# Optimization experiments

Measured on AMD Instinct MI355X. Metric: run time of the kernel, lower is better.

## Reference

```python
import jax, jax.numpy as jnp
import numpy as np

B, T, D, H, L, V = 4, 1024, 1024, 16, 6, 32000
HS = D // H
FF = 4 * D
EPS = 1e-5


def setup_inputs() -> dict:
    key = jax.random.key(0)
    ks = jax.random.split(key, 16)
    s = 0.02
    n = lambda k, shape: (jax.random.normal(k, shape, jnp.float32) * s)
    return {
        'idx': jax.random.randint(ks[0], (B, T), 0, V),
        'targets': jax.random.randint(ks[1], (B, T), 0, V),
        'tok_emb': n(ks[2], (V, D)),
        'pos_emb': n(ks[3], (T, D)),
        'Wq': n(ks[4], (L, D, H, HS)),
        'Wk': n(ks[5], (L, D, H, HS)),
        'Wv': n(ks[6], (L, D, H, HS)),
        'proj_w': n(ks[7], (L, D, D)),
        'proj_b': jnp.zeros((L, D), jnp.float32),
        'ln1_g': jnp.ones((L, D), jnp.float32),
        'ln1_b': jnp.zeros((L, D), jnp.float32),
        'ln2_g': jnp.ones((L, D), jnp.float32),
        'ln2_b': jnp.zeros((L, D), jnp.float32),
        'ff_w1': n(ks[8], (L, D, FF)),
        'ff_b1': jnp.zeros((L, FF), jnp.float32),
        'ff_w2': n(ks[9], (L, FF, D)),
        'ff_b2': jnp.zeros((L, D), jnp.float32),
        'lnf_g': jnp.ones((D,), jnp.float32),
        'lnf_b': jnp.zeros((D,), jnp.float32),
        'head_w': n(ks[10], (D, V)),
        'head_b': jnp.zeros((V,), jnp.float32),
    }


def _ln(x, g, b):
    m = jnp.mean(x, axis=-1, keepdims=True)
    v = jnp.mean((x - m) ** 2, axis=-1, keepdims=True)
    return (x - m) * jax.lax.rsqrt(v + EPS) * g + b


def _forward(idx, targets, tok_emb, pos_emb, Wq, Wk, Wv, proj_w, proj_b,
             ln1_g, ln1_b, ln2_g, ln2_b, ff_w1, ff_b1, ff_w2, ff_b2,
             lnf_g, lnf_b, head_w, head_b):
    b, t = idx.shape
    x = tok_emb[idx] + pos_emb[:t]                       # [B,T,D]
    mask = jnp.tril(jnp.ones((t, t), bool))              # causal
    scale = jnp.float32(D) ** -0.5                       # NOTE: scales by num_dims (c), as in source
    for l in range(L):
        h = _ln(x, ln1_g[l], ln1_b[l])
        q = jnp.einsum('btd,dhs->bhts', h, Wq[l])        # [B,H,T,HS]
        k = jnp.einsum('btd,dhs->bhts', h, Wk[l])
        v = jnp.einsum('btd,dhs->bhts', h, Wv[l])
        w = jnp.einsum('bhts,bhus->bhtu', q, k) * scale  # [B,H,T,T]
        w = jnp.where(mask, w, -jnp.inf)
        w = jax.nn.softmax(w, axis=-1)
        o = jnp.einsum('bhtu,bhus->bhts', w, v)          # [B,H,T,HS]
        o = o.transpose(0, 2, 1, 3).reshape(b, t, D)     # concat heads
        x = x + jnp.einsum('btd,de->bte', o, proj_w[l]) + proj_b[l]
        h2 = _ln(x, ln2_g[l], ln2_b[l])
        ff = jax.nn.relu(jnp.einsum('btd,df->btf', h2, ff_w1[l]) + ff_b1[l])
        x = x + jnp.einsum('btf,fd->btd', ff, ff_w2[l]) + ff_b2[l]
    x = _ln(x, lnf_g, lnf_b)
    logits = jnp.einsum('btd,dv->btv', x, head_w) + head_b
    logits = logits.reshape(b * t, V)
    tgt = targets.reshape(b * t)
    logp = jax.nn.log_softmax(logits, axis=-1)
    loss = -jnp.mean(jnp.take_along_axis(logp, tgt[:, None], axis=-1))
    return logits, loss


def reference(idx, targets, tok_emb, pos_emb, Wq, Wk, Wv, proj_w, proj_b,
              ln1_g, ln1_b, ln2_g, ln2_b, ff_w1, ff_b1, ff_w2, ff_b2,
              lnf_g, lnf_b, head_w, head_b):
    return _forward(idx, targets, tok_emb, pos_emb, Wq, Wk, Wv, proj_w, proj_b,
                    ln1_g, ln1_b, ln2_g, ln2_b, ff_w1, ff_b1, ff_w2, ff_b2,
                    lnf_g, lnf_b, head_w, head_b)
```

## Files before the change

### kernel.cpp

```cpp
#include <hip/hip_runtime.h>

typedef __attribute__((ext_vector_type(8))) short bf16x8;
typedef __attribute__((ext_vector_type(4))) float f32x4;

#define L_LAYERS 6
#define T_SEQ 1024
#define D_MODEL 1024
#define N_HEAD 16
#define HS 64
#define FF_DIM 4096
#define VOCAB 32000
#define BT_ROWS 4096
#define ATTN_SCALE 0.03125f

__device__ __forceinline__ ushort f2bf(float f) {
  unsigned u = __builtin_bit_cast(unsigned, f);
  unsigned r = (u + 0x7fffu + ((u >> 16) & 1u)) >> 16;
  return (ushort)r;
}
__device__ __forceinline__ float waveRedSum(float v) {
#pragma unroll
  for (int off = 32; off; off >>= 1) v += __shfl_xor(v, off);
  return v;
}
__device__ __forceinline__ void gload16(const void* g, void* l) {
  __builtin_amdgcn_global_load_lds(
      (const __attribute__((address_space(1))) unsigned int*)g,
      (__attribute__((address_space(3))) unsigned int*)l, 16, 0, 0);
}

__global__ __launch_bounds__(256) void embed_kernel(const int* __restrict__ idx,
                                                    const float* __restrict__ tok,
                                                    const float* __restrict__ pos,
                                                    float* __restrict__ x) {
  int row = blockIdx.x;
  int tid = threadIdx.x;
  int t = row & (T_SEQ - 1);
  int id = idx[row];
  float4 tv = ((const float4*)(tok + (size_t)id * D_MODEL))[tid];
  float4 pv = ((const float4*)(pos + (size_t)t * D_MODEL))[tid];
  tv.x += pv.x; tv.y += pv.y; tv.z += pv.z; tv.w += pv.w;
  ((float4*)(x + (size_t)row * D_MODEL))[tid] = tv;
}

__global__ __launch_bounds__(256) void ln_kernel(const float* __restrict__ x,
                                                 const float* __restrict__ g,
                                                 const float* __restrict__ b,
                                                 ushort* __restrict__ out) {
  int row = blockIdx.x;
  int tid = threadIdx.x;
  __shared__ float red[4];
  float4 xv = ((const float4*)(x + (size_t)row * D_MODEL))[tid];
  float s = xv.x + xv.y + xv.z + xv.w;
  s = waveRedSum(s);
  if ((tid & 63) == 0) red[tid >> 6] = s;
  __syncthreads();
  float mean = (red[0] + red[1] + red[2] + red[3]) * (1.0f / D_MODEL);
  __syncthreads();
  float d0 = xv.x - mean, d1 = xv.y - mean, d2 = xv.z - mean, d3 = xv.w - mean;
  float v = d0 * d0 + d1 * d1 + d2 * d2 + d3 * d3;
  v = waveRedSum(v);
  if ((tid & 63) == 0) red[tid >> 6] = v;
  __syncthreads();
  float var = (red[0] + red[1] + red[2] + red[3]) * (1.0f / D_MODEL);
  float rstd = rsqrtf(var + 1e-5f);
  float4 gv = ((const float4*)g)[tid];
  float4 bv = ((const float4*)b)[tid];
  ushort4 o;
  o.x = f2bf(d0 * rstd * gv.x + bv.x);
  o.y = f2bf(d1 * rstd * gv.y + bv.y);
  o.z = f2bf(d2 * rstd * gv.z + bv.z);
  o.w = f2bf(d3 * rstd * gv.w + bv.w);
  ((ushort4*)(out + (size_t)row * D_MODEL))[tid] = o;
}

__device__ __forceinline__ void wconv_body(const float* __restrict__ W,
                                           ushort* __restrict__ WT,
                                           int Kd, int Nd, int n0, int k0) {
  __shared__ ushort tile[64][72];
  int tid = threadIdx.x;
#pragma unroll
  for (int i = 0; i < 4; i++) {
    int c = tid + i * 256;
    int row = c >> 4, cc = c & 15;
    float4 wv = *(const float4*)&W[(size_t)(k0 + row) * Nd + n0 + cc * 4];
    tile[row][cc * 4 + 0] = f2bf(wv.x);
    tile[row][cc * 4 + 1] = f2bf(wv.y);
    tile[row][cc * 4 + 2] = f2bf(wv.z);
    tile[row][cc * 4 + 3] = f2bf(wv.w);
  }
  __syncthreads();
#pragma unroll
  for (int i = 0; i < 2; i++) {
    int c = tid + i * 256;
    int n = c >> 3, kc = c & 7;
    __align__(16) ushort tmp[8];
#pragma unroll
    for (int j = 0; j < 8; j++) tmp[j] = tile[kc * 8 + j][n];
    *(int4*)&WT[(size_t)(n0 + n) * Kd + k0 + kc * 8] = *(const int4*)tmp;
  }
}

__global__ __launch_bounds__(256) void wconv_kernel(const float* __restrict__ W,
                                                    ushort* __restrict__ WT,
                                                    int Kd, int Nd) {
  wconv_body(W, WT, Kd, Nd, blockIdx.x * 64, blockIdx.y * 64);
}

__global__ __launch_bounds__(256) void wconv4_kernel(const float* __restrict__ W0,
                                                     const float* __restrict__ W1,
                                                     const float* __restrict__ W2,
                                                     const float* __restrict__ W3,
                                                     ushort* __restrict__ WT,
                                                     int Kd, int Nd) {
  int z = blockIdx.z;
  const float* W = (z == 0) ? W0 : (z == 1) ? W1 : (z == 2) ? W2 : W3;
  wconv_body(W, WT + (size_t)z * Kd * Nd, Kd, Nd, blockIdx.x * 64, blockIdx.y * 64);
}

__global__ __launch_bounds__(256) void vtrans_kernel(const ushort* __restrict__ v,
                                                     ushort* __restrict__ vT) {
  __shared__ ushort tile[64][72];
  int bh = blockIdx.y;
  int t0 = blockIdx.x * 64;
  int tid = threadIdx.x;
#pragma unroll
  for (int i = 0; i < 2; i++) {
    int c = tid + i * 256;
    int row = c >> 3, cc = c & 7;
    *(int4*)&tile[row][cc * 8] =
        *(const int4*)&v[((size_t)bh * T_SEQ + t0 + row) * HS + cc * 8];
  }
  __syncthreads();
#pragma unroll
  for (int i = 0; i < 2; i++) {
    int c = tid + i * 256;
    int hs = c >> 3, tc = c & 7;
    __align__(16) ushort tmp[8];
#pragma unroll
    for (int j = 0; j < 8; j++) tmp[j] = tile[tc * 8 + j][hs];
    *(int4*)&vT[((size_t)bh * HS + hs) * T_SEQ + t0 + tc * 8] = *(const int4*)tmp;
  }
}

template <int BM, int BN, int WM, int WN, int EPI>
__global__ __launch_bounds__(WM * WN * 64, 2) void gemmp_kernel(
    const ushort* __restrict__ A, const ushort* __restrict__ BT, int K,
    const float* __restrict__ bias, float* __restrict__ outf,
    ushort* __restrict__ outb, ushort* __restrict__ outk,
    ushort* __restrict__ outv, int ldo) {
  constexpr int PM = BM / WM, PN = BN / WN;
  constexpr int MR = PM / 16, NR = PN / 16;
  constexpr int ROWS = BM + BN;
  constexpr int NWAVES = WM * WN;
  constexpr int LPW = (ROWS / 8) / NWAVES;
  __shared__ __align__(16) ushort buf[2][ROWS * 64];
  int tid = threadIdx.x;
  int lane = tid & 63, wave = tid >> 6;
  int wm = wave / WN, wn = wave % WN;
  int a = lane & 15, gg = lane >> 4;
  int srow8 = lane >> 3;
  int scol8 = ((lane & 7) ^ (lane >> 3)) * 8;
  int m0 = blockIdx.y * BM, n0 = blockIdx.x * BN;
  f32x4 acc[MR][NR] = {};
  int nt = K >> 6;

  auto STAGE = [&](int t, int d) {
    int k0 = t * 64;
#pragma unroll
    for (int j = 0; j < LPW; j++) {
      int r0 = (wave * LPW + j) * 8;
      if (r0 < BM) {
        gload16(&A[(size_t)(m0 + r0 + srow8) * K + k0 + scol8], &buf[d][r0 * 64]);
      } else {
        gload16(&BT[(size_t)(n0 + (r0 - BM) + srow8) * K + k0 + scol8], &buf[d][r0 * 64]);
      }
    }
  };

  auto COMPUTE = [&](int d) {
    const ushort* bA = &buf[d][0];
    const ushort* bB = &buf[d][BM * 64];
#pragma unroll
    for (int s = 0; s < 2; s++) {
      bf16x8 af[MR], bfr[NR];
#pragma unroll
      for (int i = 0; i < MR; i++) {
        int row = wm * PM + i * 16 + a;
        af[i] = *(const bf16x8*)&bA[row * 64 + (((s * 4 + gg) ^ (a & 7)) * 8)];
      }
#pragma unroll
      for (int j = 0; j < NR; j++) {
        int row = wn * PN + j * 16 + a;
        bfr[j] = *(const bf16x8*)&bB[row * 64 + (((s * 4 + gg) ^ (a & 7)) * 8)];
      }
#pragma unroll
      for (int i = 0; i < MR; i++)
#pragma unroll
        for (int j = 0; j < NR; j++)
          acc[i][j] = __builtin_amdgcn_mfma_f32_16x16x32_bf16(af[i], bfr[j], acc[i][j], 0, 0, 0);
    }
  };

  STAGE(0, 0);
  __syncthreads();
  int cur = 0;
  for (int t = 0; t < nt; t++) {
    if (t + 1 < nt) STAGE(t + 1, cur ^ 1);
    COMPUTE(cur);
    __syncthreads();
    cur ^= 1;
  }

#pragma unroll
  for (int i = 0; i < MR; i++) {
#pragma unroll
    for (int j = 0; j < NR; j++) {
#pragma unroll
      for (int r = 0; r < 4; r++) {
        int mrow = m0 + wm * PM + i * 16 + gg * 4 + r;
        int ncol = n0 + wn * PN + j * 16 + a;
        float v = acc[i][j][r];
        if (EPI == 0) {
          int which = ncol >> 10;
          int n1 = ncol & 1023;
          int h = n1 >> 6, sidx = n1 & 63;
          int bb = mrow >> 10, tt = mrow & 1023;
          ushort* dst = (which == 0) ? outb : (which == 1) ? outk : outv;
          dst[(((size_t)(bb * N_HEAD + h)) * T_SEQ + tt) * HS + sidx] = f2bf(v);
        } else if (EPI == 1) {
          outf[(size_t)mrow * ldo + ncol] += v + bias[ncol];
        } else if (EPI == 2) {
          float t2 = v + bias[ncol];
          outb[(size_t)mrow * ldo + ncol] = f2bf(t2 > 0.0f ? t2 : 0.0f);
        } else {
          outf[(size_t)mrow * ldo + ncol] = v + bias[ncol];
        }
      }
    }
  }
}

template <int EPI, bool SWZ>
__global__ __launch_bounds__(512, 2) void gemm8_kernel(
    const ushort* __restrict__ A, const ushort* __restrict__ BT, int K,
    const float* __restrict__ bias, float* __restrict__ outf,
    ushort* __restrict__ outb, ushort* __restrict__ outk,
    ushort* __restrict__ outv, int ldo) {
  extern __shared__ __align__(16) ushort lds[];
  int tid = threadIdx.x;
  int lane = tid & 63, wave = tid >> 6;
  int wm = wave >> 2, wn = wave & 3;
  int a = lane & 15, gg = lane >> 4;
  int bx = blockIdx.x, by = blockIdx.y;
  if (SWZ) {
    int gx = gridDim.x, nwg = gx * gridDim.y;
    int wg = by * gx + bx;
    int id = (wg & 7) * (nwg >> 3) + (wg >> 3);
    bx = id % gx; by = id / gx;
  }
  int m0 = by * 256, n0 = bx * 256;
  int srow = lane >> 3;
  int scol = ((lane & 7) ^ (lane >> 3)) * 8;
  int nt = K >> 6;
  f32x4 acc[8][4] = {};

  auto stageHalf = [&](int t, int which) {
    int d = t & 1;
    int k0 = t * 64;
    const ushort* src = (which < 2) ? A : BT;
    int base0 = ((which < 2) ? m0 : n0) + (which & 1) * 128;
    ushort* dst = lds + ((which < 2) ? 0 : 32768) + d * 16384 + (which & 1) * 8192;
#pragma unroll
    for (int q = 0; q < 2; q++) {
      int r0 = q * 64 + wave * 8;
      gload16(&src[(size_t)(base0 + r0 + srow) * K + k0 + scol], dst + r0 * 64);
    }
  };

  stageHalf(0, 0); stageHalf(0, 1); stageHalf(0, 2); stageHalf(0, 3);
  if (nt > 1) {
    stageHalf(1, 2); stageHalf(1, 3);
    asm volatile("s_waitcnt vmcnt(4)" ::: "memory");
  } else {
    asm volatile("s_waitcnt vmcnt(0)" ::: "memory");
  }
  __builtin_amdgcn_sched_barrier(0);
  __builtin_amdgcn_s_barrier();

  for (int t = 0; t < nt; t++) {
    int d = t & 1;
    const ushort* bA = lds + d * 16384;
    const ushort* bB = lds + 32768 + d * 16384;
    bf16x8 alo[4][2], ahi[4][2], bj01[2][2], bj23[2][2];
#pragma unroll
    for (int i = 0; i < 4; i++)
#pragma unroll
      for (int s = 0; s < 2; s++) {
        int row = wm * 128 + i * 16 + a;
        alo[i][s] = *(const bf16x8*)&bA[row * 64 + (((s * 4 + gg) ^ (a & 7)) * 8)];
      }
#pragma unroll
    for (int j = 0; j < 2; j++)
#pragma unroll
      for (int s = 0; s < 2; s++) {
        int row = wn * 64 + j * 16 + a;
        bj01[j][s] = *(const bf16x8*)&bB[row * 64 + (((s * 4 + gg) ^ (a & 7)) * 8)];
      }
    if (t + 1 < nt) stageHalf(t + 1, 0);
    __builtin_amdgcn_s_barrier();
    asm volatile("s_waitcnt lgkmcnt(0)" ::: "memory");
    __builtin_amdgcn_sched_barrier(0);
    __builtin_amdgcn_s_setprio(1);
#pragma unroll
    for (int i = 0; i < 4; i++)
#pragma unroll
      for (int j = 0; j < 2; j++)
#pragma unroll
        for (int s = 0; s < 2; s++)
          acc[i][j] = __builtin_amdgcn_mfma_f32_16x16x32_bf16(alo[i][s], bj01[j][s], acc[i][j], 0, 0, 0);
    __builtin_amdgcn_s_setprio(0);
    __builtin_amdgcn_s_barrier();
#pragma unroll
    for (int j = 0; j < 2; j++)
#pragma unroll
      for (int s = 0; s < 2; s++) {
        int row = wn * 64 + (j + 2) * 16 + a;
        bj23[j][s] = *(const bf16x8*)&bB[row * 64 + (((s * 4 + gg) ^ (a & 7)) * 8)];
      }
    if (t + 1 < nt) stageHalf(t + 1, 1);
    __builtin_amdgcn_s_barrier();
    asm volatile("s_waitcnt lgkmcnt(0)" ::: "memory");
    __builtin_amdgcn_sched_barrier(0);
    __builtin_amdgcn_s_setprio(1);
#pragma unroll
    for (int i = 0; i < 4; i++)
#pragma unroll
      for (int j = 0; j < 2; j++)
#pragma unroll
        for (int s = 0; s < 2; s++)
          acc[i][j + 2] = __builtin_amdgcn_mfma_f32_16x16x32_bf16(alo[i][s], bj23[j][s], acc[i][j + 2], 0, 0, 0);
    __builtin_amdgcn_s_setprio(0);
    __builtin_amdgcn_s_barrier();
#pragma unroll
    for (int i = 0; i < 4; i++)
#pragma unroll
      for (int s = 0; s < 2; s++) {
        int row = wm * 128 + (i + 4) * 16 + a;
        ahi[i][s] = *(const bf16x8*)&bA[row * 64 + (((s * 4 + gg) ^ (a & 7)) * 8)];
      }
    if (t + 2 < nt) stageHalf(t + 2, 2);
    __builtin_amdgcn_s_barrier();
    asm volatile("s_waitcnt lgkmcnt(0)" ::: "memory");
    __builtin_amdgcn_sched_barrier(0);
    __builtin_amdgcn_s_setprio(1);
#pragma unroll
    for (int i = 0; i < 4; i++)
#pragma unroll
      for (int j = 0; j < 2; j++)
#pragma unroll
        for (int s = 0; s < 2; s++)
          acc[i + 4][j] = __builtin_amdgcn_mfma_f32_16x16x32_bf16(ahi[i][s], bj01[j][s], acc[i + 4][j], 0, 0, 0);
    __builtin_amdgcn_s_setprio(0);
    __builtin_amdgcn_s_barrier();
    if (t + 2 < nt) stageHalf(t + 2, 3);
    __builtin_amdgcn_s_barrier();
    __builtin_amdgcn_s_setprio(1);
#pragma unroll
    for (int i = 0; i < 4; i++)
#pragma unroll
      for (int j = 0; j < 2; j++)
#pragma unroll
        for (int s = 0; s < 2; s++)
          acc[i + 4][j + 2] = __builtin_amdgcn_mfma_f32_16x16x32_bf16(ahi[i][s], bj23[j][s], acc[i + 4][j + 2], 0, 0, 0);
    __builtin_amdgcn_s_setprio(0);
    __builtin_amdgcn_sched_barrier(0);
    if (t + 1 < nt) {
      if (t + 2 < nt) asm volatile("s_waitcnt vmcnt(4)" ::: "memory");
      else            asm volatile("s_waitcnt vmcnt(0)" ::: "memory");
      __builtin_amdgcn_sched_barrier(0);
    }
    __builtin_amdgcn_s_barrier();
  }

#pragma unroll
  for (int i = 0; i < 8; i++) {
#pragma unroll
    for (int j = 0; j < 4; j++) {
#pragma unroll
      for (int r = 0; r < 4; r++) {
        int mrow = m0 + wm * 128 + i * 16 + gg * 4 + r;
        int ncol = n0 + wn * 64 + j * 16 + a;
        float v = acc[i][j][r];
        if (EPI == 0) {
          int which = ncol >> 10;
          int n1 = ncol & 1023;
          int h = n1 >> 6, sidx = n1 & 63;
          int bb = mrow >> 10, tt = mrow & 1023;
          ushort* dst = (which == 0) ? outb : (which == 1) ? outk : outv;
          dst[(((size_t)(bb * N_HEAD + h)) * T_SEQ + tt) * HS + sidx] = f2bf(v);
        } else if (EPI == 2) {
          float t2 = v + bias[ncol];
          outb[(size_t)mrow * ldo + ncol] = f2bf(t2 > 0.0f ? t2 : 0.0f);
        } else {
          outf[(size_t)mrow * ldo + ncol] = v + bias[ncol];
        }
      }
    }
  }
}

__global__ __launch_bounds__(256) void attn_kernel(const ushort* __restrict__ q,
                                                   const ushort* __restrict__ k,
                                                   const ushort* __restrict__ vT,
                                                   ushort* __restrict__ o) {
  __shared__ __align__(16) ushort Ksm[64 * 72];
  __shared__ __align__(16) ushort Vsm[64 * 72];
  __shared__ __align__(16) ushort Psm[4][16 * 72];
  int tid = threadIdx.x;
  int lane = tid & 63, w = tid >> 6;
  int a = lane & 15, gg = lane >> 4;
  int qt = blockIdx.x, bh = blockIdx.y;
  int qrow_b = qt * 64 + w * 16;
  int qmy = qrow_b + a;

  bf16x8 qf[2];
  const ushort* qbase = q + ((size_t)bh * T_SEQ + qmy) * HS;
  qf[0] = *(const bf16x8*)&qbase[gg * 8];
  qf[1] = *(const bf16x8*)&qbase[32 + gg * 8];

  float m_run = -__builtin_inff();
  float l_run = 0.0f;
  f32x4 oacc[4] = {};
  int nkt = qt + 1;

  for (int kt = 0; kt < nkt; kt++) {
    int k0 = kt * 64;
    __syncthreads();
#pragma unroll
    for (int i = 0; i < 2; i++) {
      int c = tid + i * 256;
      int row = c >> 3, cc = c & 7;
      *(int4*)&Ksm[row * 72 + cc * 8] =
          *(const int4*)&k[((size_t)bh * T_SEQ + k0 + row) * HS + cc * 8];
      *(int4*)&Vsm[row * 72 + cc * 8] =
          *(const int4*)&vT[((size_t)bh * HS + row) * T_SEQ + k0 + cc * 8];
    }
    __syncthreads();

    f32x4 st[4] = {};
#pragma unroll
    for (int ku = 0; ku < 4; ku++) {
#pragma unroll
      for (int s = 0; s < 2; s++) {
        bf16x8 kf = *(const bf16x8*)&Ksm[(ku * 16 + a) * 72 + s * 32 + gg * 8];
        st[ku] = __builtin_amdgcn_mfma_f32_16x16x32_bf16(kf, qf[s], st[ku], 0, 0, 0);
      }
    }

    float pv[16];
    float pm = -__builtin_inff();
#pragma unroll
    for (int ku = 0; ku < 4; ku++) {
#pragma unroll
      for (int r = 0; r < 4; r++) {
        int u = k0 + ku * 16 + gg * 4 + r;
        float val = (u <= qmy) ? st[ku][r] * ATTN_SCALE : -__builtin_inff();
        pv[ku * 4 + r] = val;
        pm = fmaxf(pm, val);
      }
    }
    pm = fmaxf(pm, __shfl_xor(pm, 16));
    pm = fmaxf(pm, __shfl_xor(pm, 32));
    float m_new = fmaxf(m_run, pm);
    float cfac = expf(m_run - m_new);
    float tsum = 0.0f;
#pragma unroll
    for (int xi = 0; xi < 16; xi++) {
      float p = expf(pv[xi] - m_new);
      pv[xi] = p;
      tsum += p;
    }
    tsum += __shfl_xor(tsum, 16);
    tsum += __shfl_xor(tsum, 32);
    l_run = l_run * cfac + tsum;
    m_run = m_new;

    ushort* P = (ushort*)&Psm[w][0];
    asm volatile("s_waitcnt lgkmcnt(0)" ::: "memory");
#pragma unroll
    for (int ku = 0; ku < 4; ku++) {
      ushort4 pw;
      pw.x = f2bf(pv[ku * 4 + 0]);
      pw.y = f2bf(pv[ku * 4 + 1]);
      pw.z = f2bf(pv[ku * 4 + 2]);
      pw.w = f2bf(pv[ku * 4 + 3]);
      *(ushort4*)&P[a * 72 + ku * 16 + gg * 4] = pw;
    }
#pragma unroll
    for (int r = 0; r < 4; r++) {
      float cr = __shfl(cfac, gg * 4 + r);
#pragma unroll
      for (int nb = 0; nb < 4; nb++) oacc[nb][r] *= cr;
    }
    asm volatile("s_waitcnt lgkmcnt(0)" ::: "memory");
#pragma unroll
    for (int kb = 0; kb < 2; kb++) {
      bf16x8 pa = *(const bf16x8*)&P[a * 72 + kb * 32 + gg * 8];
#pragma unroll
      for (int nb = 0; nb < 4; nb++) {
        bf16x8 vb = *(const bf16x8*)&Vsm[(nb * 16 + a) * 72 + kb * 32 + gg * 8];
        oacc[nb] = __builtin_amdgcn_mfma_f32_16x16x32_bf16(pa, vb, oacc[nb], 0, 0, 0);
      }
    }
  }

  float linv = 1.0f / l_run;
  int bb = bh >> 4, hh = bh & 15;
#pragma unroll
  for (int r = 0; r < 4; r++) {
    float li = __shfl(linv, gg * 4 + r);
    int qr = qrow_b + gg * 4 + r;
#pragma unroll
    for (int nb = 0; nb < 4; nb++) {
      o[((size_t)(bb * T_SEQ + qr)) * D_MODEL + hh * HS + nb * 16 + a] =
          f2bf(oacc[nb][r] * li);
    }
  }
}

__global__ __launch_bounds__(256) void loss_row_kernel(const float* __restrict__ logits,
                                                       const int* __restrict__ tgt,
                                                       float* __restrict__ row_loss) {
  int row = blockIdx.x, tid = threadIdx.x;
  __shared__ float redm[4], reds[4];
  const float4* l4 = (const float4*)(logits + (size_t)row * VOCAB);
  float m = -__builtin_inff(), s = 0.0f;
  for (int i = tid; i < VOCAB / 4; i += 256) {
    float4 v = l4[i];
    float cm = fmaxf(fmaxf(v.x, v.y), fmaxf(v.z, v.w));
    if (cm > m) { s *= expf(m - cm); m = cm; }
    s += expf(v.x - m) + expf(v.y - m) + expf(v.z - m) + expf(v.w - m);
  }
#pragma unroll
  for (int off = 32; off; off >>= 1) {
    float om = __shfl_xor(m, off), os = __shfl_xor(s, off);
    float nm = fmaxf(m, om);
    s = s * expf(m - nm) + os * expf(om - nm);
    m = nm;
  }
  if ((tid & 63) == 0) { redm[tid >> 6] = m; reds[tid >> 6] = s; }
  __syncthreads();
  if (tid == 0) {
    float M = fmaxf(fmaxf(redm[0], redm[1]), fmaxf(redm[2], redm[3]));
    float S = reds[0] * expf(redm[0] - M) + reds[1] * expf(redm[1] - M) +
              reds[2] * expf(redm[2] - M) + reds[3] * expf(redm[3] - M);
    row_loss[row] = M + logf(S) - logits[(size_t)row * VOCAB + tgt[row]];
  }
}

__global__ __launch_bounds__(256) void loss_final_kernel(const float* __restrict__ row_loss,
                                                         float* __restrict__ out) {
  int tid = threadIdx.x;
  __shared__ float red[4];
  float s = 0.0f;
  for (int i = tid; i < BT_ROWS; i += 256) s += row_loss[i];
  s = waveRedSum(s);
  if ((tid & 63) == 0) red[tid >> 6] = s;
  __syncthreads();
  if (tid == 0) out[0] = (red[0] + red[1] + red[2] + red[3]) * (1.0f / BT_ROWS);
}

extern "C" void kernel_launch(void* const* d_in, const int* in_sizes, int n_in,
                              void* d_out, int out_size, void* d_ws, size_t ws_size,
                              hipStream_t stream) {
  const int* idx = (const int*)d_in[0];
  const int* tgt = (const int*)d_in[1];
  const float* tok_emb = (const float*)d_in[2];
  const float* pos_emb = (const float*)d_in[3];
  const float* Wq = (const float*)d_in[4];
  const float* Wk = (const float*)d_in[5];
  const float* Wv = (const float*)d_in[6];
  const float* proj_w = (const float*)d_in[7];
  const float* proj_b = (const float*)d_in[8];
  const float* ln1_g = (const float*)d_in[9];
  const float* ln1_b = (const float*)d_in[10];
  const float* ln2_g = (const float*)d_in[11];
  const float* ln2_b = (const float*)d_in[12];
  const float* ff_w1 = (const float*)d_in[13];
  const float* ff_b1 = (const float*)d_in[14];
  const float* ff_w2 = (const float*)d_in[15];
  const float* ff_b2 = (const float*)d_in[16];
  const float* lnf_g = (const float*)d_in[17];
  const float* lnf_b = (const float*)d_in[18];
  const float* head_w = (const float*)d_in[19];
  const float* head_b = (const float*)d_in[20];

  char* ws = (char*)d_ws;
  size_t off = 0;
  float* x = (float*)(ws + off); off += (size_t)BT_ROWS * D_MODEL * 4;
  ushort* h = (ushort*)(ws + off); off += (size_t)BT_ROWS * D_MODEL * 2;
  ushort* qb = (ushort*)(ws + off); off += (size_t)BT_ROWS * D_MODEL * 2;
  ushort* kb = (ushort*)(ws + off); off += (size_t)BT_ROWS * D_MODEL * 2;
  ushort* vb = (ushort*)(ws + off); off += (size_t)BT_ROWS * D_MODEL * 2;
  ushort* vTb = (ushort*)(ws + off); off += (size_t)BT_ROWS * D_MODEL * 2;
  ushort* ob = (ushort*)(ws + off); off += (size_t)BT_ROWS * D_MODEL * 2;
  ushort* ffb = (ushort*)(ws + off); off += (size_t)BT_ROWS * FF_DIM * 2;
  ushort* wqkvT = (ushort*)(ws + off); off += (size_t)4 * D_MODEL * D_MODEL * 2;
  ushort* wprojT = wqkvT + (size_t)3 * D_MODEL * D_MODEL;
  ushort* wff1T = (ushort*)(ws + off); off += (size_t)FF_DIM * D_MODEL * 2;
  ushort* wff2T = (ushort*)(ws + off); off += (size_t)D_MODEL * FF_DIM * 2;
  float* row_loss = (float*)(ws + off); off += (size_t)BT_ROWS * 4;
  ushort* headT = qb;

  float* logits = (float*)d_out;

  embed_kernel<<<BT_ROWS, 256, 0, stream>>>(idx, tok_emb, pos_emb, x);

  for (int l = 0; l < L_LAYERS; l++) {
    size_t wo = (size_t)l * D_MODEL * D_MODEL;
    size_t fo = (size_t)l * D_MODEL * FF_DIM;
    wconv4_kernel<<<dim3(16, 16, 4), 256, 0, stream>>>(Wq + wo, Wk + wo, Wv + wo, proj_w + wo,
                                                       wqkvT, D_MODEL, D_MODEL);
    wconv_kernel<<<dim3(64, 16), 256, 0, stream>>>(ff_w1 + fo, wff1T, D_MODEL, FF_DIM);
    wconv_kernel<<<dim3(16, 64), 256, 0, stream>>>(ff_w2 + fo, wff2T, FF_DIM, D_MODEL);

    ln_kernel<<<BT_ROWS, 256, 0, stream>>>(x, ln1_g + l * D_MODEL, ln1_b + l * D_MODEL, h);
    gemm8_kernel<0, false><<<dim3(12, 16), 512, 131072, stream>>>(
        h, wqkvT, D_MODEL, nullptr, nullptr, qb, kb, vb, 0);
    vtrans_kernel<<<dim3(16, 64), 256, 0, stream>>>(vb, vTb);
    attn_kernel<<<dim3(16, 64), 256, 0, stream>>>(qb, kb, vTb, ob);
    gemmp_kernel<128, 128, 2, 2, 1><<<dim3(8, 32), 256, 0, stream>>>(
        ob, wprojT, D_MODEL, proj_b + l * D_MODEL, x, nullptr, nullptr, nullptr, D_MODEL);
    ln_kernel<<<BT_ROWS, 256, 0, stream>>>(x, ln2_g + l * D_MODEL, ln2_b + l * D_MODEL, h);
    gemm8_kernel<2, false><<<dim3(16, 16), 512, 131072, stream>>>(
        h, wff1T, D_MODEL, ff_b1 + (size_t)l * FF_DIM, nullptr, ffb, nullptr, nullptr, FF_DIM);
    gemmp_kernel<128, 128, 2, 2, 1><<<dim3(8, 32), 256, 0, stream>>>(
        ffb, wff2T, FF_DIM, ff_b2 + l * D_MODEL, x, nullptr, nullptr, nullptr, D_MODEL);
  }

  ln_kernel<<<BT_ROWS, 256, 0, stream>>>(x, lnf_g, lnf_b, h);

  wconv_kernel<<<dim3(500, 16), 256, 0, stream>>>(head_w, headT, D_MODEL, VOCAB);
  gemm8_kernel<3, true><<<dim3(125, 16), 512, 131072, stream>>>(
      h, headT, D_MODEL, head_b, logits, nullptr, nullptr, nullptr, VOCAB);

  loss_row_kernel<<<BT_ROWS, 256, 0, stream>>>(logits, tgt, row_loss);
  loss_final_kernel<<<1, 256, 0, stream>>>(row_loss, logits + (size_t)BT_ROWS * VOCAB);
}
```

Before: 2.067 ms.

## Fuse log-sum-exp partials into LM head GEMM epilogue and shrink loss kernel

The head GEMM epilogue now computes a per-row partial max and sum-of-exp over its 256-column tile, reduced through shuffles and LDS, and writes them to a small partials buffer. The loss kernel then combines 125 partials per row instead of rereading the full 4096x32000 fp32 logits tensor. The swizzled tile mapping is also changed to walk along M first within a column group. This adds exp work and an LDS reduction to the GEMM epilogue in exchange for removing a large memory pass.

Result: slower. 2.119 ms (+2.5%).

```diff
diff --git a/kernel.cpp b/kernel.cpp
--- a/kernel.cpp
+++ b/kernel.cpp
@@ -246,7 +246,7 @@
     const ushort* __restrict__ A, const ushort* __restrict__ BT, int K,
     const float* __restrict__ bias, float* __restrict__ outf,
     ushort* __restrict__ outb, ushort* __restrict__ outk,
-    ushort* __restrict__ outv, int ldo) {
+    ushort* __restrict__ outv, int ldo, float2* __restrict__ part) {
   extern __shared__ __align__(16) ushort lds[];
   int tid = threadIdx.x;
   int lane = tid & 63, wave = tid >> 6;
@@ -254,10 +254,11 @@
   int a = lane & 15, gg = lane >> 4;
   int bx = blockIdx.x, by = blockIdx.y;
   if (SWZ) {
-    int gx = gridDim.x, nwg = gx * gridDim.y;
+    int gx = gridDim.x, gy = gridDim.y;
+    int nwg = gx * gy;
     int wg = by * gx + bx;
     int id = (wg & 7) * (nwg >> 3) + (wg >> 3);
-    bx = id % gx; by = id / gx;
+    by = id % gy; bx = id / gy;
   }
   int m0 = by * 256, n0 = bx * 256;
   int srow = lane >> 3;
@@ -381,6 +382,64 @@
       __builtin_amdgcn_sched_barrier(0);
     }
     __builtin_amdgcn_s_barrier();
+  }
+
+  if (EPI == 3) {
+    float bj[4];
+#pragma unroll
+    for (int j = 0; j < 4; j++) bj[j] = bias[n0 + wn * 64 + j * 16 + a];
+#pragma unroll
+    for (int i = 0; i < 8; i++)
+#pragma unroll
+      for (int j = 0; j < 4; j++)
+#pragma unroll
+        for (int r = 0; r < 4; r++) acc[i][j][r] += bj[j];
+#pragma unroll
+    for (int i = 0; i < 8; i++)
+#pragma unroll
+      for (int j = 0; j < 4; j++)
+#pragma unroll
+        for (int r = 0; r < 4; r++) {
+          int mrow = m0 + wm * 128 + i * 16 + gg * 4 + r;
+          int ncol = n0 + wn * 64 + j * 16 + a;
+          outf[(size_t)mrow * ldo + ncol] = acc[i][j][r];
+        }
+    float2* sm = (float2*)lds;
+#pragma unroll
+    for (int i = 0; i < 8; i++) {
+#pragma unroll
+      for (int r = 0; r < 4; r++) {
+        float pm = fmaxf(fmaxf(acc[i][0][r], acc[i][1][r]),
+                         fmaxf(acc[i][2][r], acc[i][3][r]));
+        float ps = expf(acc[i][0][r] - pm) + expf(acc[i][1][r] - pm) +
+                   expf(acc[i][2][r] - pm) + expf(acc[i][3][r] - pm);
+#pragma unroll
+        for (int off = 1; off < 16; off <<= 1) {
+          float om = __shfl_xor(pm, off), os = __shfl_xor(ps, off);
+          float nm = fmaxf(pm, om);
+          ps = ps * expf(pm - nm) + os * expf(om - nm);
+          pm = nm;
+        }
+        if (a == 0) {
+          float2 v2; v2.x = pm; v2.y = ps;
+          sm[(wm * 128 + i * 16 + gg * 4 + r) * 4 + wn] = v2;
+        }
+      }
+    }
+    __syncthreads();
+    if (tid < 256) {
+      float m = -__builtin_inff(), s = 0.0f;
+#pragma unroll
+      for (int w4 = 0; w4 < 4; w4++) {
+        float2 p = sm[tid * 4 + w4];
+        float nm = fmaxf(m, p.x);
+        s = s * expf(m - nm) + p.y * expf(p.x - nm);
+        m = nm;
+      }
+      float2 o2; o2.x = m; o2.y = s;
+      part[(size_t)(m0 + tid) * 128 + (n0 >> 8)] = o2;
+    }
+    return;
   }
 
 #pragma unroll
@@ -402,8 +461,6 @@
         } else if (EPI == 2) {
           float t2 = v + bias[ncol];
           outb[(size_t)mrow * ldo + ncol] = f2bf(t2 > 0.0f ? t2 : 0.0f);
-        } else {
-          outf[(size_t)mrow * ldo + ncol] = v + bias[ncol];
         }
       }
     }
@@ -529,34 +586,32 @@
   }
 }
 
-__global__ __launch_bounds__(256) void loss_row_kernel(const float* __restrict__ logits,
+__global__ __launch_bounds__(64) void loss_rows_kernel(const float2* __restrict__ part,
+                                                       const float* __restrict__ logits,
                                                        const int* __restrict__ tgt,
                                                        float* __restrict__ row_loss) {
-  int row = blockIdx.x, tid = threadIdx.x;
-  __shared__ float redm[4], reds[4];
-  const float4* l4 = (const float4*)(logits + (size_t)row * VOCAB);
+  int row = blockIdx.x;
+  int l = threadIdx.x;
   float m = -__builtin_inff(), s = 0.0f;
-  for (int i = tid; i < VOCAB / 4; i += 256) {
-    float4 v = l4[i];
-    float cm = fmaxf(fmaxf(v.x, v.y), fmaxf(v.z, v.w));
-    if (cm > m) { s *= expf(m - cm); m = cm; }
-    s += expf(v.x - m) + expf(v.y - m) + expf(v.z - m) + expf(v.w - m);
-  }
-#pragma unroll
-  for (int off = 32; off; off >>= 1) {
+#pragma unroll
+  for (int q = 0; q < 2; q++) {
+    int c = l * 2 + q;
+    if (c < 125) {
+      float2 p = part[(size_t)row * 128 + c];
+      float nm = fmaxf(m, p.x);
+      s = s * expf(m - nm) + p.y * expf(p.x - nm);
+      m = nm;
+    }
+  }
+#pragma unroll
+  for (int off = 1; off < 64; off <<= 1) {
     float om = __shfl_xor(m, off), os = __shfl_xor(s, off);
     float nm = fmaxf(m, om);
     s = s * expf(m - nm) + os * expf(om - nm);
     m = nm;
   }
-  if ((tid & 63) == 0) { redm[tid >> 6] = m; reds[tid >> 6] = s; }
-  __syncthreads();
-  if (tid == 0) {
-    float M = fmaxf(fmaxf(redm[0], redm[1]), fmaxf(redm[2], redm[3]));
-    float S = reds[0] * expf(redm[0] - M) + reds[1] * expf(redm[1] - M) +
-              reds[2] * expf(redm[2] - M) + reds[3] * expf(redm[3] - M);
-    row_loss[row] = M + logf(S) - logits[(size_t)row * VOCAB + tgt[row]];
-  }
+  if (l == 0)
+    row_loss[row] = m + logf(s) - logits[(size_t)row * VOCAB + tgt[row]];
 }
 
 __global__ __launch_bounds__(256) void loss_final_kernel(const float* __restrict__ row_loss,
@@ -611,6 +666,7 @@
   ushort* wff1T = (ushort*)(ws + off); off += (size_t)FF_DIM * D_MODEL * 2;
   ushort* wff2T = (ushort*)(ws + off); off += (size_t)D_MODEL * FF_DIM * 2;
   float* row_loss = (float*)(ws + off); off += (size_t)BT_ROWS * 4;
+  float2* part = (float2*)(ws + off); off += (size_t)BT_ROWS * 128 * 8;
   ushort* headT = qb;
 
   float* logits = (float*)d_out;
@@ -627,14 +683,15 @@
 
     ln_kernel<<<BT_ROWS, 256, 0, stream>>>(x, ln1_g + l * D_MODEL, ln1_b + l * D_MODEL, h);
     gemm8_kernel<0, false><<<dim3(12, 16), 512, 131072, stream>>>(
-        h, wqkvT, D_MODEL, nullptr, nullptr, qb, kb, vb, 0);
+        h, wqkvT, D_MODEL, nullptr, nullptr, qb, kb, vb, 0, nullptr);
     vtrans_kernel<<<dim3(16, 64), 256, 0, stream>>>(vb, vTb);
     attn_kernel<<<dim3(16, 64), 256, 0, stream>>>(qb, kb, vTb, ob);
     gemmp_kernel<128, 128, 2, 2, 1><<<dim3(8, 32), 256, 0, stream>>>(
         ob, wprojT, D_MODEL, proj_b + l * D_MODEL, x, nullptr, nullptr, nullptr, D_MODEL);
     ln_kernel<<<BT_ROWS, 256, 0, stream>>>(x, ln2_g + l * D_MODEL, ln2_b + l * D_MODEL, h);
     gemm8_kernel<2, false><<<dim3(16, 16), 512, 131072, stream>>>(
-        h, wff1T, D_MODEL, ff_b1 + (size_t)l * FF_DIM, nullptr, ffb, nullptr, nullptr, FF_DIM);
+        h, wff1T, D_MODEL, ff_b1 + (size_t)l * FF_DIM, nullptr, ffb, nullptr, nullptr,
+        FF_DIM, nullptr);
     gemmp_kernel<128, 128, 2, 2, 1><<<dim3(8, 32), 256, 0, stream>>>(
         ffb, wff2T, FF_DIM, ff_b2 + l * D_MODEL, x, nullptr, nullptr, nullptr, D_MODEL);
   }
@@ -643,8 +700,8 @@
 
   wconv_kernel<<<dim3(500, 16), 256, 0, stream>>>(head_w, headT, D_MODEL, VOCAB);
   gemm8_kernel<3, true><<<dim3(125, 16), 512, 131072, stream>>>(
-      h, headT, D_MODEL, head_b, logits, nullptr, nullptr, nullptr, VOCAB);
-
-  loss_row_kernel<<<BT_ROWS, 256, 0, stream>>>(logits, tgt, row_loss);
+      h, headT, D_MODEL, head_b, logits, nullptr, nullptr, nullptr, VOCAB, part);
+
+  loss_rows_kernel<<<BT_ROWS, 64, 0, stream>>>(part, logits, tgt, row_loss);
   loss_final_kernel<<<1, 256, 0, stream>>>(row_loss, logits + (size_t)BT_ROWS * VOCAB);
 }
```
